# Optimization experiments

Hardware: AMD Instinct MI355X
Metric: run time of the kernel (lower is better)

Reference implementation:

```python
import jax, jax.numpy as jnp
import numpy as np

RES = 0.16      # config.resolution (m)
XMIN = -51.2    # config.x_min
YMIN = -51.2    # config.y_min
EPS = 1e-5      # BatchNorm eps
NEG = -1.0e9


def setup_inputs() -> dict:
    key = jax.random.key(0)
    ks = jax.random.split(key, 12)
    P, M = 100000, 32
    C_IN, C_MID, C_OUT = 9, 64, 64
    pillars = jax.random.normal(ks[0], (P, M, 4), dtype=jnp.float32)
    pillar_coords = jax.random.randint(ks[1], (P, 2), 0, 640, dtype=jnp.int64)
    num_points_per_pillar = jax.random.randint(ks[2], (P,), 0, 33, dtype=jnp.int64)
    # MLP params (Linear stored as (in,out) for x @ W + b)
    W1 = jax.random.normal(ks[3], (C_IN, C_MID), dtype=jnp.float32) / np.sqrt(C_IN)
    b1 = jax.random.normal(ks[4], (C_MID,), dtype=jnp.float32) * 0.01
    g1 = jnp.ones((C_MID,), jnp.float32)
    beta1 = jnp.zeros((C_MID,), jnp.float32)
    m1 = jax.random.normal(ks[5], (C_MID,), dtype=jnp.float32) * 0.1
    v1 = jax.random.uniform(ks[6], (C_MID,), dtype=jnp.float32, minval=0.5, maxval=1.5)
    W2 = jax.random.normal(ks[7], (C_MID, C_OUT), dtype=jnp.float32) / np.sqrt(C_MID)
    b2 = jax.random.normal(ks[8], (C_OUT,), dtype=jnp.float32) * 0.01
    g2 = jnp.ones((C_OUT,), jnp.float32)
    beta2 = jnp.zeros((C_OUT,), jnp.float32)
    m2 = jax.random.normal(ks[9], (C_OUT,), dtype=jnp.float32) * 0.1
    v2 = jax.random.uniform(ks[10], (C_OUT,), dtype=jnp.float32, minval=0.5, maxval=1.5)
    return {
        "pillars": pillars, "pillar_coords": pillar_coords,
        "num_points_per_pillar": num_points_per_pillar,
        "W1": W1, "b1": b1, "g1": g1, "beta1": beta1, "m1": m1, "v1": v1,
        "W2": W2, "b2": b2, "g2": g2, "beta2": beta2, "m2": m2, "v2": v2,
    }


def reference(pillars, pillar_coords, num_points_per_pillar,
              W1, b1, g1, beta1, m1, v1, W2, b2, g2, beta2, m2, v2):
    P, M, _ = pillars.shape
    # pillar centers from grid indices
    xc = (pillar_coords[:, 1].astype(jnp.float32) + 0.5) * RES + XMIN  # (P,)
    yc = (pillar_coords[:, 0].astype(jnp.float32) + 0.5) * RES + YMIN  # (P,)
    npts = num_points_per_pillar.astype(jnp.float32)
    mask = (jnp.arange(M)[None, :] < num_points_per_pillar[:, None]).astype(pillars.dtype)  # (P,M)
    x, y, z, r = pillars[:, :, 0], pillars[:, :, 1], pillars[:, :, 2], pillars[:, :, 3]
    z_mean = (z * mask).sum(axis=1) / jnp.clip(npts, 1.0)  # (P,)
    xo = x - xc[:, None]
    yo = y - yc[:, None]
    zo = z - z_mean[:, None]
    feat = jnp.stack([x, y, z, r, xo, yo, zo, xo, yo], axis=-1)  # (P,M,9)
    # shared MLP: Linear -> BN(eval) -> ReLU, twice
    h = feat @ W1 + b1
    h = jax.nn.relu(g1 * (h - m1) * jax.lax.rsqrt(v1 + EPS) + beta1)
    h = h @ W2 + b2
    h = jax.nn.relu(g2 * (h - m2) * jax.lax.rsqrt(v2 + EPS) + beta2)  # (P,M,64)
    # masked max over points per pillar
    m3 = mask[:, :, None]
    h = h * m3 + (1.0 - m3) * NEG
    return h.max(axis=1)  # (P,64)
```

## Files before the change

kernel.cpp:

```cpp
#include <hip/hip_runtime.h>
#include <type_traits>

#define RES_ 0.16f
#define XMIN_ -51.2f
#define YMIN_ -51.2f
#define EPS_ 1e-5f
#define NEG_ -1000000000.0f

#define WPB 4

typedef _Float16 f16x8 __attribute__((ext_vector_type(8)));
typedef _Float16 f16x4 __attribute__((ext_vector_type(4)));
typedef _Float16 f16x2 __attribute__((ext_vector_type(2)));
typedef float f32x4 __attribute__((ext_vector_type(4)));

union F8u { f16x8 v; f16x2 h[4]; };
union F4u { f16x4 v; f16x2 h[2]; };

#if __has_builtin(__builtin_amdgcn_mfma_f32_16x16x16f16)
#define MFMA1_K16 1
#else
#define MFMA1_K16 0
#endif

static __device__ __forceinline__ f16x2 pkrtz(float a, float b) {
    return __builtin_bit_cast(f16x2, __builtin_amdgcn_cvt_pkrtz(a, b));
}

static __device__ __forceinline__ f16x2 relu2(f16x2 x) {
#if __has_builtin(__builtin_elementwise_max)
    const f16x2 z2 = (f16x2)(_Float16)0.f;
    return __builtin_elementwise_max(x, z2);
#else
    f16x2 r;
    r[0] = x[0] > (_Float16)0.f ? x[0] : (_Float16)0.f;
    r[1] = x[1] > (_Float16)0.f ? x[1] : (_Float16)0.f;
    return r;
#endif
}

__global__ __launch_bounds__(256, 4) void pfn_kernel(
    const float* __restrict__ pillars,
    const int* __restrict__ coords,
    const int* __restrict__ npts_arr,
    const float* __restrict__ W1, const float* __restrict__ b1,
    const float* __restrict__ g1, const float* __restrict__ beta1,
    const float* __restrict__ m1, const float* __restrict__ v1,
    const float* __restrict__ W2, const float* __restrict__ b2,
    const float* __restrict__ g2, const float* __restrict__ beta2,
    const float* __restrict__ m2, const float* __restrict__ v2,
    float* __restrict__ out, int P)
{
    __shared__ float pts[WPB][32][4];
    __shared__ __align__(16) _Float16 h1s[WPB][32][72];

    const int tid  = threadIdx.x;
    const int wave = tid >> 6;
    const int lane = tid & 63;
    const int quad = lane >> 4;
    const int col  = lane & 15;

    float c1v[4], w16v[4];
#if MFMA1_K16
    f16x4 bw1[4];
#else
    f16x8 bw1[4];
#endif
#pragma unroll
    for (int nt = 0; nt < 4; ++nt) {
        const int n0 = nt * 16 + col;
        const float a1 = g1[n0] * rsqrtf(v1[n0] + EPS_);
        c1v[nt]  = fmaf(a1, b1[n0] - m1[n0], beta1[n0]);
        w16v[nt] = a1 * W1[6 * 64 + n0];
#if MFMA1_K16
#pragma unroll
        for (int j = 0; j < 4; ++j) {
            const int k = quad * 4 + j;
            bw1[nt][j] = (k < 9) ? (_Float16)(a1 * W1[k * 64 + n0]) : (_Float16)0.f;
        }
#else
#pragma unroll
        for (int j = 0; j < 8; ++j) {
            const int k = quad * 8 + j;
            bw1[nt][j] = (k < 9) ? (_Float16)(a1 * W1[k * 64 + n0]) : (_Float16)0.f;
        }
#endif
    }

    f16x8 bw2[2][4];
#pragma unroll
    for (int nt = 0; nt < 4; ++nt) {
        const int n0 = nt * 16 + col;
        const float a2 = g2[n0] * rsqrtf(v2[n0] + EPS_);
#pragma unroll
        for (int kt = 0; kt < 2; ++kt)
#pragma unroll
            for (int j = 0; j < 8; ++j) {
                const int phys = kt * 32 + quad * 8 + j;
                const int orig = (phys & 3) * 16 + (phys >> 2);
                bw2[kt][nt][j] = (_Float16)(a2 * W2[orig * 64 + n0]);
            }
    }
    const float a2o   = g2[lane] * rsqrtf(v2[lane] + EPS_);
    const float c2own = fmaf(a2o, b2[lane] - m2[lane], beta2[lane]);

    const int nwaves = gridDim.x * WPB;
    int p = __builtin_amdgcn_readfirstlane(blockIdx.x * WPB + wave);
    if (p >= P) return;

    float2 pv = ((const float2*)(pillars + (size_t)p * 128))[lane];
    int np = npts_arr[p];
    int cy = coords[2 * p], cx = coords[2 * p + 1];

    while (true) {
        const int pn = p + nwaves;
        const bool has_next = pn < P;
        float2 pvn; int npn = 0, cyn = 0, cxn = 0;
        if (has_next) {
            pvn = ((const float2*)(pillars + (size_t)pn * 128))[lane];
            npn = npts_arr[pn];
            cyn = coords[2 * pn]; cxn = coords[2 * pn + 1];
        }

        np = np < 0 ? 0 : (np > 32 ? 32 : np);
        const int npu = __builtin_amdgcn_readfirstlane(np);
        const float xc = ((float)cx + 0.5f) * RES_ + XMIN_;
        const float yc = ((float)cy + 0.5f) * RES_ + YMIN_;

        ((float2*)&pts[wave][0][0])[lane] = pv;

        float zv = ((lane & 1) && ((lane >> 1) < np)) ? pv.x : 0.0f;
#pragma unroll
        for (int off = 1; off <= 32; off <<= 1) zv += __shfl_xor(zv, off, 64);
        const float z_mean = zv / fmaxf((float)np, 1.0f);

        __threadfence_block();

        auto body = [&](auto MTC) -> float {
            constexpr int MT = decltype(MTC)::value;

#if MFMA1_K16
            f16x4 av1[MT];
#else
            f16x8 av1[MT];
#endif
#pragma unroll
            for (int mt = 0; mt < MT; ++mt) {
                const float4 pt = *(const float4*)&pts[wave][mt * 16 + col][0];
                const float xo = pt.x - xc;
                const float yo = pt.y - yc;
                const f16x2 c01 = pkrtz(pt.x, pt.y);
                const f16x2 c23 = pkrtz(pt.z, pt.w);
                const f16x2 c45 = pkrtz(xo, yo);
                const f16x2 c67 = pkrtz(pt.z, xo);
                const f16x2 c89 = pkrtz(yo, 0.0f);
                const f16x2 z2  = (f16x2)(_Float16)0.f;
#if MFMA1_K16
                F4u u;
                u.h[0] = (quad == 0) ? c01 : (quad == 1) ? c45 : (quad == 2) ? c89 : z2;
                u.h[1] = (quad == 0) ? c23 : (quad == 1) ? c67 : z2;
                av1[mt] = u.v;
#else
                F8u u;
                u.h[0] = (quad == 0) ? c01 : (quad == 1) ? c89 : z2;
                u.h[1] = (quad == 0) ? c23 : z2;
                u.h[2] = (quad == 0) ? c45 : z2;
                u.h[3] = (quad == 0) ? c67 : z2;
                av1[mt] = u.v;
#endif
            }

            f32x4 acc1[MT][4];
#pragma unroll
            for (int nt = 0; nt < 4; ++nt) {
                const float ci = fmaf(-z_mean, w16v[nt], c1v[nt]);
                const f32x4 cinit = {ci, ci, ci, ci};
#pragma unroll
                for (int mt = 0; mt < MT; ++mt)
#if MFMA1_K16
                    acc1[mt][nt] = __builtin_amdgcn_mfma_f32_16x16x16f16(av1[mt], bw1[nt], cinit, 0, 0, 0);
#else
                    acc1[mt][nt] = __builtin_amdgcn_mfma_f32_16x16x32_f16(av1[mt], bw1[nt], cinit, 0, 0, 0);
#endif
            }

#pragma unroll
            for (int mt = 0; mt < MT; ++mt)
#pragma unroll
                for (int r = 0; r < 4; ++r) {
                    const int m = mt * 16 + quad * 4 + r;
                    F4u w;
                    w.h[0] = relu2(pkrtz(acc1[mt][0][r], acc1[mt][1][r]));
                    w.h[1] = relu2(pkrtz(acc1[mt][2][r], acc1[mt][3][r]));
                    *(f16x4*)&h1s[wave][m][col * 4] = w.v;
                }
            __threadfence_block();

            f16x8 a2f[MT][2];
#pragma unroll
            for (int mt = 0; mt < MT; ++mt)
#pragma unroll
                for (int kt = 0; kt < 2; ++kt)
                    a2f[mt][kt] = *(const f16x8*)&h1s[wave][mt * 16 + col][kt * 32 + quad * 8];

            f32x4 cm[MT];
#pragma unroll
            for (int mt = 0; mt < MT; ++mt)
#pragma unroll
                for (int r = 0; r < 4; ++r)
                    cm[mt][r] = (mt * 16 + quad * 4 + r < np) ? 0.0f : NEG_;

            float hmv[4];
#pragma unroll
            for (int nt = 0; nt < 4; ++nt) {
                f32x4 acc[MT];
#pragma unroll
                for (int mt = 0; mt < MT; ++mt) {
                    acc[mt] = __builtin_amdgcn_mfma_f32_16x16x32_f16(a2f[mt][0], bw2[0][nt], cm[mt], 0, 0, 0);
                    acc[mt] = __builtin_amdgcn_mfma_f32_16x16x32_f16(a2f[mt][1], bw2[1][nt], acc[mt], 0, 0, 0);
                }
                float hm = fmaxf(fmaxf(acc[0][0], acc[0][1]), fmaxf(acc[0][2], acc[0][3]));
                if (MT == 2) {
                    const float t1 = fmaxf(fmaxf(acc[MT - 1][0], acc[MT - 1][1]),
                                           fmaxf(acc[MT - 1][2], acc[MT - 1][3]));
                    hm = fmaxf(hm, t1);
                }
                hm = fmaxf(hm, __shfl_xor(hm, 16, 64));
                hm = fmaxf(hm, __shfl_xor(hm, 32, 64));
                hmv[nt] = hm;
            }
            float r0 = (quad == 0) ? hmv[0] : (quad == 1) ? hmv[1] : (quad == 2) ? hmv[2] : hmv[3];
            return fmaxf(r0 + c2own, 0.0f);
        };

        float res;
        if (npu > 16)     res = body(std::integral_constant<int, 2>{});
        else if (npu > 0) res = body(std::integral_constant<int, 1>{});
        else              res = NEG_;
        out[(size_t)p * 64 + lane] = res;

        if (!has_next) break;
        p = pn; pv = pvn; np = npn; cy = cyn; cx = cxn;
    }
}

extern "C" void kernel_launch(void* const* d_in, const int* in_sizes, int n_in,
                              void* d_out, int out_size, void* d_ws, size_t ws_size,
                              hipStream_t stream) {
    const float* pillars = (const float*)d_in[0];
    const int*   coords  = (const int*)d_in[1];
    const int*   npts    = (const int*)d_in[2];
    const float* W1      = (const float*)d_in[3];
    const float* b1      = (const float*)d_in[4];
    const float* g1      = (const float*)d_in[5];
    const float* beta1   = (const float*)d_in[6];
    const float* m1      = (const float*)d_in[7];
    const float* v1      = (const float*)d_in[8];
    const float* W2      = (const float*)d_in[9];
    const float* b2      = (const float*)d_in[10];
    const float* g2      = (const float*)d_in[11];
    const float* beta2   = (const float*)d_in[12];
    const float* m2      = (const float*)d_in[13];
    const float* v2      = (const float*)d_in[14];
    float* out           = (float*)d_out;

    const int P = in_sizes[2];
    const int blocks = 1024;

    hipLaunchKernelGGL(pfn_kernel, dim3(blocks), dim3(256), 0, stream,
                       pillars, coords, npts, W1, b1, g1, beta1, m1, v1,
                       W2, b2, g2, beta2, m2, v2, out, P);
}
```

Measured before the change: 153.6 us.

## Transpose layer-1 MFMA so outputs feed layer-2 from registers, dropping LDS staging

Layer 1 now computes the transposed product (weights as the A operand, points as B), so each lane's accumulator fragment already matches the A-operand layout of the second MFMA, and W2 rows are permuted to match. This removes the shared-memory round trip for both the point data and the hidden activations, along with the associated fences. Bias and the z-mean term are folded into extra K columns (a constant 1 and -z_mean), and points are loaded directly as float4 per lane. The z-mean term is now carried in fp16, which reduces its precision, and each lane issues duplicated point loads across quads.

New measurement: 151.3 us. Within noise of the previous version (-1.5%).

```diff
diff --git a/kernel.cpp b/kernel.cpp
--- a/kernel.cpp
+++ b/kernel.cpp
@@ -16,12 +16,6 @@
 
 union F8u { f16x8 v; f16x2 h[4]; };
 union F4u { f16x4 v; f16x2 h[2]; };
-
-#if __has_builtin(__builtin_amdgcn_mfma_f32_16x16x16f16)
-#define MFMA1_K16 1
-#else
-#define MFMA1_K16 0
-#endif
 
 static __device__ __forceinline__ f16x2 pkrtz(float a, float b) {
     return __builtin_bit_cast(f16x2, __builtin_amdgcn_cvt_pkrtz(a, b));
@@ -51,40 +45,28 @@
     const float* __restrict__ m2, const float* __restrict__ v2,
     float* __restrict__ out, int P)
 {
-    __shared__ float pts[WPB][32][4];
-    __shared__ __align__(16) _Float16 h1s[WPB][32][72];
-
     const int tid  = threadIdx.x;
     const int wave = tid >> 6;
     const int lane = tid & 63;
     const int quad = lane >> 4;
     const int col  = lane & 15;
 
-    float c1v[4], w16v[4];
-#if MFMA1_K16
-    f16x4 bw1[4];
-#else
-    f16x8 bw1[4];
-#endif
-#pragma unroll
-    for (int nt = 0; nt < 4; ++nt) {
-        const int n0 = nt * 16 + col;
-        const float a1 = g1[n0] * rsqrtf(v1[n0] + EPS_);
-        c1v[nt]  = fmaf(a1, b1[n0] - m1[n0], beta1[n0]);
-        w16v[nt] = a1 * W1[6 * 64 + n0];
-#if MFMA1_K16
+    f16x4 aw1[4];
+#pragma unroll
+    for (int mt = 0; mt < 4; ++mt) {
+        const int ch = mt * 16 + col;
+        const float a1 = g1[ch] * rsqrtf(v1[ch] + EPS_);
+        const float c1 = fmaf(a1, b1[ch] - m1[ch], beta1[ch]);
 #pragma unroll
         for (int j = 0; j < 4; ++j) {
             const int k = quad * 4 + j;
-            bw1[nt][j] = (k < 9) ? (_Float16)(a1 * W1[k * 64 + n0]) : (_Float16)0.f;
+            float w;
+            if (k < 9)       w = a1 * W1[k * 64 + ch];
+            else if (k == 9)  w = c1;
+            else if (k == 10) w = a1 * W1[6 * 64 + ch];
+            else              w = 0.0f;
+            aw1[mt][j] = (_Float16)w;
         }
-#else
-#pragma unroll
-        for (int j = 0; j < 8; ++j) {
-            const int k = quad * 8 + j;
-            bw1[nt][j] = (k < 9) ? (_Float16)(a1 * W1[k * 64 + n0]) : (_Float16)0.f;
-        }
-#endif
     }
 
     f16x8 bw2[2][4];
@@ -96,28 +78,31 @@
         for (int kt = 0; kt < 2; ++kt)
 #pragma unroll
             for (int j = 0; j < 8; ++j) {
-                const int phys = kt * 32 + quad * 8 + j;
-                const int orig = (phys & 3) * 16 + (phys >> 2);
-                bw2[kt][nt][j] = (_Float16)(a2 * W2[orig * 64 + n0]);
+                const int c = 32 * kt + 16 * (j >> 2) + 4 * quad + (j & 3);
+                bw2[kt][nt][j] = (_Float16)(a2 * W2[c * 64 + n0]);
             }
     }
-    const float a2o   = g2[lane] * rsqrtf(v2[lane] + EPS_);
-    const float c2own = fmaf(a2o, b2[lane] - m2[lane], beta2[lane]);
+    const float c2own = fmaf(g2[lane] * rsqrtf(v2[lane] + EPS_),
+                             b2[lane] - m2[lane], beta2[lane]);
 
     const int nwaves = gridDim.x * WPB;
     int p = __builtin_amdgcn_readfirstlane(blockIdx.x * WPB + wave);
     if (p >= P) return;
 
-    float2 pv = ((const float2*)(pillars + (size_t)p * 128))[lane];
+    const float4* pb = (const float4*)(pillars + (size_t)p * 128);
+    float4 ptA = pb[col];
+    float4 ptB = pb[16 + col];
     int np = npts_arr[p];
     int cy = coords[2 * p], cx = coords[2 * p + 1];
 
     while (true) {
         const int pn = p + nwaves;
         const bool has_next = pn < P;
-        float2 pvn; int npn = 0, cyn = 0, cxn = 0;
+        float4 ptAn, ptBn; int npn = 0, cyn = 0, cxn = 0;
         if (has_next) {
-            pvn = ((const float2*)(pillars + (size_t)pn * 128))[lane];
+            const float4* pbn = (const float4*)(pillars + (size_t)pn * 128);
+            ptAn = pbn[col];
+            ptBn = pbn[16 + col];
             npn = npts_arr[pn];
             cyn = coords[2 * pn]; cxn = coords[2 * pn + 1];
         }
@@ -127,104 +112,69 @@
         const float xc = ((float)cx + 0.5f) * RES_ + XMIN_;
         const float yc = ((float)cy + 0.5f) * RES_ + YMIN_;
 
-        ((float2*)&pts[wave][0][0])[lane] = pv;
-
-        float zv = ((lane & 1) && ((lane >> 1) < np)) ? pv.x : 0.0f;
-#pragma unroll
-        for (int off = 1; off <= 32; off <<= 1) zv += __shfl_xor(zv, off, 64);
-        const float z_mean = zv / fmaxf((float)np, 1.0f);
-
-        __threadfence_block();
+        float zs = (col < np) ? ptA.z : 0.0f;
+        zs += (16 + col < np) ? ptB.z : 0.0f;
+#pragma unroll
+        for (int off = 1; off <= 8; off <<= 1) zs += __shfl_xor(zs, off, 64);
+        const float z_mean = zs / fmaxf((float)np, 1.0f);
 
         auto body = [&](auto MTC) -> float {
             constexpr int MT = decltype(MTC)::value;
-
-#if MFMA1_K16
-            f16x4 av1[MT];
-#else
-            f16x8 av1[MT];
-#endif
-#pragma unroll
-            for (int mt = 0; mt < MT; ++mt) {
-                const float4 pt = *(const float4*)&pts[wave][mt * 16 + col][0];
+            float hm4[4] = {NEG_, NEG_, NEG_, NEG_};
+
+#pragma unroll
+            for (int t = 0; t < MT; ++t) {
+                const float4 pt = (t == 0) ? ptA : ptB;
+
                 const float xo = pt.x - xc;
                 const float yo = pt.y - yc;
                 const f16x2 c01 = pkrtz(pt.x, pt.y);
                 const f16x2 c23 = pkrtz(pt.z, pt.w);
                 const f16x2 c45 = pkrtz(xo, yo);
                 const f16x2 c67 = pkrtz(pt.z, xo);
-                const f16x2 c89 = pkrtz(yo, 0.0f);
+                const f16x2 c89 = pkrtz(yo, 1.0f);
+                const f16x2 cab = pkrtz(-z_mean, 0.0f);
                 const f16x2 z2  = (f16x2)(_Float16)0.f;
-#if MFMA1_K16
                 F4u u;
                 u.h[0] = (quad == 0) ? c01 : (quad == 1) ? c45 : (quad == 2) ? c89 : z2;
-                u.h[1] = (quad == 0) ? c23 : (quad == 1) ? c67 : z2;
-                av1[mt] = u.v;
-#else
-                F8u u;
-                u.h[0] = (quad == 0) ? c01 : (quad == 1) ? c89 : z2;
-                u.h[1] = (quad == 0) ? c23 : z2;
-                u.h[2] = (quad == 0) ? c45 : z2;
-                u.h[3] = (quad == 0) ? c67 : z2;
-                av1[mt] = u.v;
-#endif
+                u.h[1] = (quad == 0) ? c23 : (quad == 1) ? c67 : (quad == 2) ? cab : z2;
+                const f16x4 bt = u.v;
+
+                f32x4 acc1[4];
+                const f32x4 zz = {0.f, 0.f, 0.f, 0.f};
+#pragma unroll
+                for (int mt = 0; mt < 4; ++mt)
+                    acc1[mt] = __builtin_amdgcn_mfma_f32_16x16x16f16(aw1[mt], bt, zz, 0, 0, 0);
+
+                f16x8 av2[2];
+#pragma unroll
+                for (int kt = 0; kt < 2; ++kt) {
+                    F8u w;
+                    w.h[0] = relu2(pkrtz(acc1[2 * kt][0],     acc1[2 * kt][1]));
+                    w.h[1] = relu2(pkrtz(acc1[2 * kt][2],     acc1[2 * kt][3]));
+                    w.h[2] = relu2(pkrtz(acc1[2 * kt + 1][0], acc1[2 * kt + 1][1]));
+                    w.h[3] = relu2(pkrtz(acc1[2 * kt + 1][2], acc1[2 * kt + 1][3]));
+                    av2[kt] = w.v;
+                }
+
+                f32x4 cm;
+#pragma unroll
+                for (int r = 0; r < 4; ++r)
+                    cm[r] = (t * 16 + quad * 4 + r < np) ? 0.0f : NEG_;
+
+#pragma unroll
+                for (int nt = 0; nt < 4; ++nt) {
+                    f32x4 acc = __builtin_amdgcn_mfma_f32_16x16x32_f16(av2[0], bw2[0][nt], cm, 0, 0, 0);
+                    acc = __builtin_amdgcn_mfma_f32_16x16x32_f16(av2[1], bw2[1][nt], acc, 0, 0, 0);
+                    const float tmax = fmaxf(fmaxf(acc[0], acc[1]), fmaxf(acc[2], acc[3]));
+                    hm4[nt] = fmaxf(hm4[nt], tmax);
+                }
             }
 
-            f32x4 acc1[MT][4];
+            float hmv[4];
 #pragma unroll
             for (int nt = 0; nt < 4; ++nt) {
-                const float ci = fmaf(-z_mean, w16v[nt], c1v[nt]);
-                const f32x4 cinit = {ci, ci, ci, ci};
-#pragma unroll
-                for (int mt = 0; mt < MT; ++mt)
-#if MFMA1_K16
-                    acc1[mt][nt] = __builtin_amdgcn_mfma_f32_16x16x16f16(av1[mt], bw1[nt], cinit, 0, 0, 0);
-#else
-                    acc1[mt][nt] = __builtin_amdgcn_mfma_f32_16x16x32_f16(av1[mt], bw1[nt], cinit, 0, 0, 0);
-#endif
-            }
-
-#pragma unroll
-            for (int mt = 0; mt < MT; ++mt)
-#pragma unroll
-                for (int r = 0; r < 4; ++r) {
-                    const int m = mt * 16 + quad * 4 + r;
-                    F4u w;
-                    w.h[0] = relu2(pkrtz(acc1[mt][0][r], acc1[mt][1][r]));
-                    w.h[1] = relu2(pkrtz(acc1[mt][2][r], acc1[mt][3][r]));
-                    *(f16x4*)&h1s[wave][m][col * 4] = w.v;
-                }
-            __threadfence_block();
-
-            f16x8 a2f[MT][2];
-#pragma unroll
-            for (int mt = 0; mt < MT; ++mt)
-#pragma unroll
-                for (int kt = 0; kt < 2; ++kt)
-                    a2f[mt][kt] = *(const f16x8*)&h1s[wave][mt * 16 + col][kt * 32 + quad * 8];
-
-            f32x4 cm[MT];
-#pragma unroll
-            for (int mt = 0; mt < MT; ++mt)
-#pragma unroll
-                for (int r = 0; r < 4; ++r)
-                    cm[mt][r] = (mt * 16 + quad * 4 + r < np) ? 0.0f : NEG_;
-
-            float hmv[4];
-#pragma unroll
-            for (int nt = 0; nt < 4; ++nt) {
-                f32x4 acc[MT];
-#pragma unroll
-                for (int mt = 0; mt < MT; ++mt) {
-                    acc[mt] = __builtin_amdgcn_mfma_f32_16x16x32_f16(a2f[mt][0], bw2[0][nt], cm[mt], 0, 0, 0);
-                    acc[mt] = __builtin_amdgcn_mfma_f32_16x16x32_f16(a2f[mt][1], bw2[1][nt], acc[mt], 0, 0, 0);
-                }
-                float hm = fmaxf(fmaxf(acc[0][0], acc[0][1]), fmaxf(acc[0][2], acc[0][3]));
-                if (MT == 2) {
-                    const float t1 = fmaxf(fmaxf(acc[MT - 1][0], acc[MT - 1][1]),
-                                           fmaxf(acc[MT - 1][2], acc[MT - 1][3]));
-                    hm = fmaxf(hm, t1);
-                }
+                float hm = hm4[nt];
                 hm = fmaxf(hm, __shfl_xor(hm, 16, 64));
                 hm = fmaxf(hm, __shfl_xor(hm, 32, 64));
                 hmv[nt] = hm;
@@ -240,7 +190,7 @@
         out[(size_t)p * 64 + lane] = res;
 
         if (!has_next) break;
-        p = pn; pv = pvn; np = npn; cy = cyn; cx = cxn;
+        p = pn; ptA = ptAn; ptB = ptBn; np = npn; cy = cyn; cx = cxn;
     }
 }
 
```
